# Performance work log

Hardware: AMD Instinct MI355X
Metric: run time of the kernel (lower is better)

## Reference

```python
import jax, jax.numpy as jnp
import numpy as np

B, C, H, W = 64, 3, 256, 256
K = 2  # multi_n_num
EPS_NORM = 1e-8
EPS_DEN = 1e-7
SCALE = 0.01


def setup_inputs() -> dict:
    key = jax.random.key(0)
    ka, kp, kn, kj = jax.random.split(key, 4)
    a = jax.random.normal(ka, (B, C, H, W), dtype=jnp.float32)
    p = jax.random.normal(kp, (B, C, H, W), dtype=jnp.float32)
    n = jax.random.normal(kn, (B, C, H, W), dtype=jnp.float32)
    # sample_with_j(B, 2, i) -> [i, random j != i]
    ar = jnp.arange(B, dtype=jnp.int64)
    off = jax.random.randint(kj, (B,), 1, B)  # offset in [1, B) guarantees j != i
    neg_idx = jnp.stack([ar, (ar + off) % B], axis=1).astype(jnp.int64)  # [B, K]
    return {"a": a, "p": p, "n": n, "neg_idx": neg_idx}


def _fft_norm(x):
    # torch.fft.fft2 over last two dims -> complex, same rank as x
    f = jnp.fft.fft2(x, axes=(-2, -1))  # [B, C, H, W] complex64
    # torch.norm(f, p=2, dim=1, keepdim=True) on complex = sqrt(sum |f|^2 over C)
    nrm = jnp.sqrt(jnp.sum(jnp.abs(f) ** 2, axis=1, keepdims=True))
    return f / (nrm + EPS_NORM) * SCALE


def reference(a, p, n, neg_idx):
    af = _fft_norm(a)
    pf = _fft_norm(p)
    nf = _fft_norm(n)
    # L1Loss on complex tensors = mean |diff| (complex magnitude)
    d_ap = jnp.mean(jnp.abs(af - pf), axis=(1, 2, 3))  # [B]
    n_sel = nf[neg_idx]  # [B, K, C, H, W]
    d_an = jnp.mean(jnp.abs(af[:, None] - n_sel), axis=(2, 3, 4))  # [B, K]
    contrastive = jnp.sum(d_ap[:, None] / (d_an + EPS_DEN))
    return contrastive / (K * B)
```

## Files before the change

kernel.cpp:

```cpp
#include <hip/hip_runtime.h>
#include <hip/hip_fp16.h>

#define B_ 64
#define SW_ 132
#define SIMG_ (256 * SW_)
#define TIMG_ (3 * SIMG_)
#define TELEMS_ ((size_t)B_ * TIMG_)
#define SST_ 257

__device__ __forceinline__ float2 h2f(__half2 v) { return __half22float2(v); }
__device__ __forceinline__ __half2 f2h(float2 v) { return __float22half2_rn(v); }
__device__ __forceinline__ float2 cmul(float2 a, float2 b) {
  return make_float2(a.x * b.x - a.y * b.y, a.x * b.y + a.y * b.x);
}
__device__ __forceinline__ int PHI(int e) { return e ^ ((e >> 4) & 0x0C); }
__device__ __forceinline__ int REV4(int k) {
  return ((k & 3) << 6) | ((k & 0xC) << 2) | ((k >> 2) & 0xC) | ((k >> 6) & 3);
}
#define LGKM0 asm volatile("s_waitcnt lgkmcnt(0)" ::: "memory")

__device__ __forceinline__ void r4stage(__half2* w, int i0, int q,
                                        float2 ta, float2 tb, float2 tc, bool tw) {
  int p0 = PHI(i0), p1 = PHI(i0 + q), p2 = PHI(i0 + 2 * q), p3 = PHI(i0 + 3 * q);
  float2 x0 = h2f(w[p0]), x1 = h2f(w[p1]), x2 = h2f(w[p2]), x3 = h2f(w[p3]);
  float2 a = make_float2(x0.x + x2.x, x0.y + x2.y);
  float2 b = make_float2(x0.x - x2.x, x0.y - x2.y);
  float2 c = make_float2(x1.x + x3.x, x1.y + x3.y);
  float2 d = make_float2(x1.x - x3.x, x1.y - x3.y);
  float2 y0 = make_float2(a.x + c.x, a.y + c.y);
  float2 y1 = make_float2(b.x + d.y, b.y - d.x);
  float2 y2 = make_float2(a.x - c.x, a.y - c.y);
  float2 y3 = make_float2(b.x - d.y, b.y + d.x);
  if (tw) { y1 = cmul(y1, ta); y2 = cmul(y2, tb); y3 = cmul(y3, tc); }
  w[p0] = f2h(y0); w[p1] = f2h(y1); w[p2] = f2h(y2); w[p3] = f2h(y3);
}

__device__ __forceinline__ void fft256_r4(__half2* w, int r, const float2* tws) {
  LGKM0;
  r4stage(w, r, 64, tws[0], tws[1], tws[2], true);
  LGKM0;
  r4stage(w, ((r >> 4) << 6) | (r & 15), 16, tws[3], tws[4], tws[5], true);
  LGKM0;
  r4stage(w, ((r >> 2) << 4) | (r & 3), 4, tws[6], tws[7], tws[8], true);
  LGKM0;
  float2 u = make_float2(1.0f, 0.0f);
  r4stage(w, 4 * r, 1, u, u, u, false);
  LGKM0;
}

__global__ __launch_bounds__(1024, 4) void fft2_fused(const float* __restrict__ a,
                                                      const float* __restrict__ p,
                                                      const float* __restrict__ n,
                                                      __half2* __restrict__ outbase) {
  __shared__ __half2 S[129 * SST_];
  __shared__ __half2 scr[16 * 256];

  int tid = threadIdx.x;
  int wv = tid >> 6;
  int r = tid & 63;
  int tensor = blockIdx.x / 192;
  int plane = blockIdx.x % 192;
  const float* in = (tensor == 0 ? a : (tensor == 1 ? p : n)) + (size_t)plane * 65536;
  __half2* outp = outbase + (size_t)tensor * TELEMS_ + (size_t)plane * SIMG_;

  float2 tw[9];
  {
    float s, c;
    __sincosf(-6.283185307179586f * (float)r / 256.0f, &s, &c);
    tw[0] = make_float2(c, s); tw[1] = cmul(tw[0], tw[0]); tw[2] = cmul(tw[1], tw[0]);
    __sincosf(-6.283185307179586f * (float)(r & 15) / 64.0f, &s, &c);
    tw[3] = make_float2(c, s); tw[4] = cmul(tw[3], tw[3]); tw[5] = cmul(tw[4], tw[3]);
    __sincosf(-6.283185307179586f * (float)(r & 3) / 16.0f, &s, &c);
    tw[6] = make_float2(c, s); tw[7] = cmul(tw[6], tw[6]); tw[8] = cmul(tw[7], tw[6]);
  }

  __half2* w = scr + wv * 256;

  for (int it = 0; it < 8; ++it) {
    int q = it * 16 + wv;
    const float4* r0 = (const float4*)(in + (size_t)(2 * q) * 256);
    const float4* r1 = (const float4*)(in + (size_t)(2 * q + 1) * 256);
    float4 v0 = r0[r];
    float4 v1 = r1[r];
    int pb = PHI(4 * r);
    w[pb]     = f2h(make_float2(v0.x, v1.x));
    w[pb + 1] = f2h(make_float2(v0.y, v1.y));
    w[pb + 2] = f2h(make_float2(v0.z, v1.z));
    w[pb + 3] = f2h(make_float2(v0.w, v1.w));
    fft256_r4(w, r, tw);
#pragma unroll
    for (int t = 0; t < 2; ++t) {
      int k = r + 64 * t;
      float2 Zk = h2f(w[PHI(REV4(k))]);
      float2 Zm = h2f(w[PHI(REV4((256 - k) & 255))]);
      float2 A  = make_float2(0.5f * (Zk.x + Zm.x), 0.5f * (Zk.y - Zm.y));
      float2 Bv = make_float2(0.5f * (Zk.y + Zm.y), 0.5f * (Zm.x - Zk.x));
      __half2* srow = S + k * SST_ + PHI(2 * q);
      srow[0] = f2h(A);
      srow[1] = f2h(Bv);
    }
    if (r == 0) {
      float2 Z = h2f(w[PHI(REV4(128))]);
      __half2* srow = S + 128 * SST_ + PHI(2 * q);
      srow[0] = f2h(make_float2(Z.x, 0.0f));
      srow[1] = f2h(make_float2(Z.y, 0.0f));
    }
    LGKM0;
  }

  __syncthreads();

  for (int it = 0; it < 9; ++it) {
    int c = it * 16 + wv;
    if (c <= 128) {
      __half2* row = S + c * SST_;
      fft256_r4(row, r, tw);
      __half2* dst = outp + (size_t)c * 256;
#pragma unroll
      for (int t = 0; t < 4; ++t) {
        int i = r + 64 * t;
        dst[i] = row[PHI(i)];
      }
    } else if (c < SW_) {
      __half2* dst = outp + (size_t)c * 256;
      __half2 z = f2h(make_float2(0.0f, 0.0f));
#pragma unroll
      for (int t = 0; t < 4; ++t) dst[r + 64 * t] = z;
    }
  }
}

__device__ __forceinline__ float cab2(float2 v) { return v.x * v.x + v.y * v.y; }

__global__ __launch_bounds__(256) void dist_kernel(const __half2* __restrict__ af,
                                                   const __half2* __restrict__ pf,
                                                   const __half2* __restrict__ nf,
                                                   const int* __restrict__ neg,
                                                   float* __restrict__ acc) {
  int b = blockIdx.y;
  int j;
  if (neg[1] == 0) {
    j = (int)((const long long*)neg)[b * 2 + 1];
  } else {
    j = neg[b * 2 + 1];
  }
  size_t ab = (size_t)b * TIMG_;
  size_t jb = (size_t)j * TIMG_;
  float s_ap = 0.0f, s_a0 = 0.0f, s_a1 = 0.0f;
#pragma unroll
  for (int t = 0; t < 4; ++t) {
    int flat = blockIdx.x * 1024 + t * 256 + threadIdx.x;
    int k2 = flat >> 8;
    float w = (k2 == 0 || k2 >= 128) ? 1.0f : 2.0f;
    float2 a0 = h2f(af[ab + flat]);
    float2 a1 = h2f(af[ab + SIMG_ + flat]);
    float2 a2 = h2f(af[ab + 2 * SIMG_ + flat]);
    float2 p0 = h2f(pf[ab + flat]);
    float2 p1 = h2f(pf[ab + SIMG_ + flat]);
    float2 p2 = h2f(pf[ab + 2 * SIMG_ + flat]);
    float2 n0 = h2f(nf[ab + flat]);
    float2 n1 = h2f(nf[ab + SIMG_ + flat]);
    float2 n2 = h2f(nf[ab + 2 * SIMG_ + flat]);
    float2 m0 = h2f(nf[jb + flat]);
    float2 m1 = h2f(nf[jb + SIMG_ + flat]);
    float2 m2 = h2f(nf[jb + 2 * SIMG_ + flat]);
    float sa = 0.01f / (sqrtf(cab2(a0) + cab2(a1) + cab2(a2)) + 1e-8f);
    float sp = 0.01f / (sqrtf(cab2(p0) + cab2(p1) + cab2(p2)) + 1e-8f);
    float sn = 0.01f / (sqrtf(cab2(n0) + cab2(n1) + cab2(n2)) + 1e-8f);
    float sm = 0.01f / (sqrtf(cab2(m0) + cab2(m1) + cab2(m2)) + 1e-8f);
    float dx, dy;
    dx = a0.x * sa - p0.x * sp; dy = a0.y * sa - p0.y * sp; s_ap += w * sqrtf(dx * dx + dy * dy);
    dx = a1.x * sa - p1.x * sp; dy = a1.y * sa - p1.y * sp; s_ap += w * sqrtf(dx * dx + dy * dy);
    dx = a2.x * sa - p2.x * sp; dy = a2.y * sa - p2.y * sp; s_ap += w * sqrtf(dx * dx + dy * dy);
    dx = a0.x * sa - n0.x * sn; dy = a0.y * sa - n0.y * sn; s_a0 += w * sqrtf(dx * dx + dy * dy);
    dx = a1.x * sa - n1.x * sn; dy = a1.y * sa - n1.y * sn; s_a0 += w * sqrtf(dx * dx + dy * dy);
    dx = a2.x * sa - n2.x * sn; dy = a2.y * sa - n2.y * sn; s_a0 += w * sqrtf(dx * dx + dy * dy);
    dx = a0.x * sa - m0.x * sm; dy = a0.y * sa - m0.y * sm; s_a1 += w * sqrtf(dx * dx + dy * dy);
    dx = a1.x * sa - m1.x * sm; dy = a1.y * sa - m1.y * sm; s_a1 += w * sqrtf(dx * dx + dy * dy);
    dx = a2.x * sa - m2.x * sm; dy = a2.y * sa - m2.y * sm; s_a1 += w * sqrtf(dx * dx + dy * dy);
  }
#pragma unroll
  for (int off = 32; off > 0; off >>= 1) {
    s_ap += __shfl_down(s_ap, off);
    s_a0 += __shfl_down(s_a0, off);
    s_a1 += __shfl_down(s_a1, off);
  }
  __shared__ float red[3][4];
  int lane = threadIdx.x & 63, wid = threadIdx.x >> 6;
  if (lane == 0) { red[0][wid] = s_ap; red[1][wid] = s_a0; red[2][wid] = s_a1; }
  __syncthreads();
  if (threadIdx.x == 0) {
    atomicAdd(&acc[b * 3 + 0], red[0][0] + red[0][1] + red[0][2] + red[0][3]);
    atomicAdd(&acc[b * 3 + 1], red[1][0] + red[1][1] + red[1][2] + red[1][3]);
    atomicAdd(&acc[b * 3 + 2], red[2][0] + red[2][1] + red[2][2] + red[2][3]);
  }
}

__global__ void zero_acc(float* acc) { acc[threadIdx.x] = 0.0f; }

__global__ void final_kernel(const float* __restrict__ acc, float* __restrict__ out) {
  int b = threadIdx.x;
  const float inv = 1.0f / 196608.0f;
  float dap = acc[b * 3 + 0] * inv;
  float da0 = acc[b * 3 + 1] * inv;
  float da1 = acc[b * 3 + 2] * inv;
  float term = dap / (da0 + 1e-7f) + dap / (da1 + 1e-7f);
#pragma unroll
  for (int off = 32; off > 0; off >>= 1) term += __shfl_down(term, off);
  if (b == 0) out[0] = term * (1.0f / 128.0f);
}

extern "C" void kernel_launch(void* const* d_in, const int* in_sizes, int n_in,
                              void* d_out, int out_size, void* d_ws, size_t ws_size,
                              hipStream_t stream) {
  const float* a = (const float*)d_in[0];
  const float* p = (const float*)d_in[1];
  const float* n = (const float*)d_in[2];
  const int* neg = (const int*)d_in[3];
  float* out = (float*)d_out;

  __half2* base = (__half2*)d_ws;
  float* acc = (float*)(base + 3 * TELEMS_);

  zero_acc<<<1, 192, 0, stream>>>(acc);
  fft2_fused<<<576, 1024, 0, stream>>>(a, p, n, base);
  dist_kernel<<<dim3(33, 64), 256, 0, stream>>>(base, base + TELEMS_,
                                                base + 2 * TELEMS_, neg, acc);
  final_kernel<<<1, 64, 0, stream>>>(acc, out);
}
```

Baseline: 253.5 us.

## Move 256-point FFT butterflies into registers with cross-lane shuffle exchanges

Replaces the LDS-scratch radix-4 FFT, which used per-stage shared-memory round trips and lgkmcnt waits, with a register-resident FFT: each lane holds four values and digit exchanges happen through __shfl_xor. The real-pair unpacking uses a shuffle to fetch mirrored bins instead of LDS reads, and the column pass stores outputs with 128-bit writes in natural order. The distance kernel now does vectorized uint4 loads of four consecutive bins per thread. Shuffles still go through the LDS crossbar, and the extra half/float conversions between stages add ALU work.

```diff
diff --git a/kernel.cpp b/kernel.cpp
--- a/kernel.cpp
+++ b/kernel.cpp
@@ -8,52 +8,73 @@
 #define TELEMS_ ((size_t)B_ * TIMG_)
 #define SST_ 257
 
-__device__ __forceinline__ float2 h2f(__half2 v) { return __half22float2(v); }
-__device__ __forceinline__ __half2 f2h(float2 v) { return __float22half2_rn(v); }
 __device__ __forceinline__ float2 cmul(float2 a, float2 b) {
   return make_float2(a.x * b.x - a.y * b.y, a.x * b.y + a.y * b.x);
 }
-__device__ __forceinline__ int PHI(int e) { return e ^ ((e >> 4) & 0x0C); }
-__device__ __forceinline__ int REV4(int k) {
-  return ((k & 3) << 6) | ((k & 0xC) << 2) | ((k >> 2) & 0xC) | ((k >> 6) & 3);
-}
-#define LGKM0 asm volatile("s_waitcnt lgkmcnt(0)" ::: "memory")
-
-__device__ __forceinline__ void r4stage(__half2* w, int i0, int q,
-                                        float2 ta, float2 tb, float2 tc, bool tw) {
-  int p0 = PHI(i0), p1 = PHI(i0 + q), p2 = PHI(i0 + 2 * q), p3 = PHI(i0 + 3 * q);
-  float2 x0 = h2f(w[p0]), x1 = h2f(w[p1]), x2 = h2f(w[p2]), x3 = h2f(w[p3]);
-  float2 a = make_float2(x0.x + x2.x, x0.y + x2.y);
-  float2 b = make_float2(x0.x - x2.x, x0.y - x2.y);
-  float2 c = make_float2(x1.x + x3.x, x1.y + x3.y);
-  float2 d = make_float2(x1.x - x3.x, x1.y - x3.y);
-  float2 y0 = make_float2(a.x + c.x, a.y + c.y);
+__device__ __forceinline__ unsigned f2u(float2 v) {
+  __half2 h = __float22half2_rn(v);
+  return __builtin_bit_cast(unsigned, h);
+}
+__device__ __forceinline__ float2 u2f(unsigned u) {
+  return __half22float2(__builtin_bit_cast(__half2, u));
+}
+
+__device__ __forceinline__ void bfly4(float2 x[4], float2 ta, float2 tb, float2 tc, bool tw) {
+  float2 a = make_float2(x[0].x + x[2].x, x[0].y + x[2].y);
+  float2 b = make_float2(x[0].x - x[2].x, x[0].y - x[2].y);
+  float2 c = make_float2(x[1].x + x[3].x, x[1].y + x[3].y);
+  float2 d = make_float2(x[1].x - x[3].x, x[1].y - x[3].y);
   float2 y1 = make_float2(b.x + d.y, b.y - d.x);
   float2 y2 = make_float2(a.x - c.x, a.y - c.y);
   float2 y3 = make_float2(b.x - d.y, b.y + d.x);
+  x[0] = make_float2(a.x + c.x, a.y + c.y);
   if (tw) { y1 = cmul(y1, ta); y2 = cmul(y2, tb); y3 = cmul(y3, tc); }
-  w[p0] = f2h(y0); w[p1] = f2h(y1); w[p2] = f2h(y2); w[p3] = f2h(y3);
-}
-
-__device__ __forceinline__ void fft256_r4(__half2* w, int r, const float2* tws) {
-  LGKM0;
-  r4stage(w, r, 64, tws[0], tws[1], tws[2], true);
-  LGKM0;
-  r4stage(w, ((r >> 4) << 6) | (r & 15), 16, tws[3], tws[4], tws[5], true);
-  LGKM0;
-  r4stage(w, ((r >> 2) << 4) | (r & 3), 4, tws[6], tws[7], tws[8], true);
-  LGKM0;
-  float2 u = make_float2(1.0f, 0.0f);
-  r4stage(w, 4 * r, 1, u, u, u, false);
-  LGKM0;
+  x[1] = y1; x[2] = y2; x[3] = y3;
+}
+
+__device__ __forceinline__ void xbit(unsigned& A, unsigned& B, int bit, int r) {
+  bool hi = (r >> bit) & 1;
+  int send = hi ? (int)A : (int)B;
+  int got = __shfl_xor(send, 1 << bit, 64);
+  if (hi) A = (unsigned)got; else B = (unsigned)got;
+}
+__device__ __forceinline__ void xdigit(unsigned u[4], int bit, int r) {
+  xbit(u[0], u[1], bit, r);
+  xbit(u[2], u[3], bit, r);
+  xbit(u[0], u[2], bit + 1, r);
+  xbit(u[1], u[3], bit + 1, r);
+}
+
+__device__ __forceinline__ void fft256_reg(float2 x[4], unsigned u[4], int r,
+                                           const float2 tw[9]) {
+  bfly4(x, tw[0], tw[1], tw[2], true);
+#pragma unroll
+  for (int s = 0; s < 4; ++s) u[s] = f2u(x[s]);
+  xdigit(u, 4, r);
+#pragma unroll
+  for (int s = 0; s < 4; ++s) x[s] = u2f(u[s]);
+  bfly4(x, tw[3], tw[4], tw[5], true);
+#pragma unroll
+  for (int s = 0; s < 4; ++s) u[s] = f2u(x[s]);
+  xdigit(u, 2, r);
+#pragma unroll
+  for (int s = 0; s < 4; ++s) x[s] = u2f(u[s]);
+  bfly4(x, tw[6], tw[7], tw[8], true);
+#pragma unroll
+  for (int s = 0; s < 4; ++s) u[s] = f2u(x[s]);
+  xdigit(u, 0, r);
+#pragma unroll
+  for (int s = 0; s < 4; ++s) x[s] = u2f(u[s]);
+  bfly4(x, tw[0], tw[0], tw[0], false);
+#pragma unroll
+  for (int s = 0; s < 4; ++s) u[s] = f2u(x[s]);
 }
 
 __global__ __launch_bounds__(1024, 4) void fft2_fused(const float* __restrict__ a,
                                                       const float* __restrict__ p,
                                                       const float* __restrict__ n,
-                                                      __half2* __restrict__ outbase) {
-  __shared__ __half2 S[129 * SST_];
-  __shared__ __half2 scr[16 * 256];
+                                                      unsigned* __restrict__ outbase) {
+  __shared__ unsigned S[129 * SST_];
 
   int tid = threadIdx.x;
   int wv = tid >> 6;
@@ -61,7 +82,7 @@
   int tensor = blockIdx.x / 192;
   int plane = blockIdx.x % 192;
   const float* in = (tensor == 0 ? a : (tensor == 1 ? p : n)) + (size_t)plane * 65536;
-  __half2* outp = outbase + (size_t)tensor * TELEMS_ + (size_t)plane * SIMG_;
+  unsigned* outp = outbase + (size_t)tensor * TELEMS_ + (size_t)plane * SIMG_;
 
   float2 tw[9];
   {
@@ -73,39 +94,36 @@
     __sincosf(-6.283185307179586f * (float)(r & 3) / 16.0f, &s, &c);
     tw[6] = make_float2(c, s); tw[7] = cmul(tw[6], tw[6]); tw[8] = cmul(tw[7], tw[6]);
   }
-
-  __half2* w = scr + wv * 256;
+  int m = ((r & 3) << 4) | (((r >> 2) & 3) << 2) | (r >> 4);
+  int mp = (64 - m) & 63;
+  int rp = ((mp >> 4) & 3) | (((mp >> 2) & 3) << 2) | ((mp & 3) << 4);
 
   for (int it = 0; it < 8; ++it) {
     int q = it * 16 + wv;
-    const float4* r0 = (const float4*)(in + (size_t)(2 * q) * 256);
-    const float4* r1 = (const float4*)(in + (size_t)(2 * q + 1) * 256);
-    float4 v0 = r0[r];
-    float4 v1 = r1[r];
-    int pb = PHI(4 * r);
-    w[pb]     = f2h(make_float2(v0.x, v1.x));
-    w[pb + 1] = f2h(make_float2(v0.y, v1.y));
-    w[pb + 2] = f2h(make_float2(v0.z, v1.z));
-    w[pb + 3] = f2h(make_float2(v0.w, v1.w));
-    fft256_r4(w, r, tw);
-#pragma unroll
-    for (int t = 0; t < 2; ++t) {
-      int k = r + 64 * t;
-      float2 Zk = h2f(w[PHI(REV4(k))]);
-      float2 Zm = h2f(w[PHI(REV4((256 - k) & 255))]);
+    const float* r0 = in + (size_t)(2 * q) * 256;
+    float2 x[4]; unsigned u[4];
+#pragma unroll
+    for (int j = 0; j < 4; ++j)
+      x[j] = make_float2(r0[r + 64 * j], r0[256 + r + 64 * j]);
+    fft256_reg(x, u, r, tw);
+    unsigned mir[4];
+#pragma unroll
+    for (int t = 0; t < 4; ++t) mir[t] = (unsigned)__shfl((int)u[t], rp, 64);
+#pragma unroll
+    for (int s = 0; s < 2; ++s) {
+      int k = 64 * s + m;
+      int sp = (m == 0) ? ((4 - s) & 3) : (3 - s);
+      float2 Zk = u2f(u[s]), Zm = u2f(mir[sp]);
       float2 A  = make_float2(0.5f * (Zk.x + Zm.x), 0.5f * (Zk.y - Zm.y));
       float2 Bv = make_float2(0.5f * (Zk.y + Zm.y), 0.5f * (Zm.x - Zk.x));
-      __half2* srow = S + k * SST_ + PHI(2 * q);
-      srow[0] = f2h(A);
-      srow[1] = f2h(Bv);
+      S[k * SST_ + 2 * q]     = f2u(A);
+      S[k * SST_ + 2 * q + 1] = f2u(Bv);
     }
     if (r == 0) {
-      float2 Z = h2f(w[PHI(REV4(128))]);
-      __half2* srow = S + 128 * SST_ + PHI(2 * q);
-      srow[0] = f2h(make_float2(Z.x, 0.0f));
-      srow[1] = f2h(make_float2(Z.y, 0.0f));
+      float2 Zk = u2f(u[2]);
+      S[128 * SST_ + 2 * q]     = f2u(make_float2(Zk.x, 0.0f));
+      S[128 * SST_ + 2 * q + 1] = f2u(make_float2(Zk.y, 0.0f));
     }
-    LGKM0;
   }
 
   __syncthreads();
@@ -113,72 +131,68 @@
   for (int it = 0; it < 9; ++it) {
     int c = it * 16 + wv;
     if (c <= 128) {
-      __half2* row = S + c * SST_;
-      fft256_r4(row, r, tw);
-      __half2* dst = outp + (size_t)c * 256;
-#pragma unroll
-      for (int t = 0; t < 4; ++t) {
-        int i = r + 64 * t;
-        dst[i] = row[PHI(i)];
-      }
-    } else if (c < SW_) {
-      __half2* dst = outp + (size_t)c * 256;
-      __half2 z = f2h(make_float2(0.0f, 0.0f));
-#pragma unroll
-      for (int t = 0; t < 4; ++t) dst[r + 64 * t] = z;
+      unsigned* srow = S + c * SST_;
+      float2 x[4]; unsigned u[4];
+#pragma unroll
+      for (int j = 0; j < 4; ++j) x[j] = u2f(srow[r + 64 * j]);
+      fft256_reg(x, u, r, tw);
+      *(uint4*)(outp + (size_t)c * 256 + 4 * r) = make_uint4(u[0], u[1], u[2], u[3]);
     }
   }
+  if (wv >= 13) {
+    int c = 129 + (wv - 13);
+    *(uint4*)(outp + (size_t)c * 256 + 4 * r) = make_uint4(0, 0, 0, 0);
+  }
 }
 
 __device__ __forceinline__ float cab2(float2 v) { return v.x * v.x + v.y * v.y; }
 
-__global__ __launch_bounds__(256) void dist_kernel(const __half2* __restrict__ af,
-                                                   const __half2* __restrict__ pf,
-                                                   const __half2* __restrict__ nf,
+__global__ __launch_bounds__(256) void dist_kernel(const unsigned* __restrict__ af,
+                                                   const unsigned* __restrict__ pf,
+                                                   const unsigned* __restrict__ nf,
                                                    const int* __restrict__ neg,
                                                    float* __restrict__ acc) {
   int b = blockIdx.y;
-  int j;
-  if (neg[1] == 0) {
-    j = (int)((const long long*)neg)[b * 2 + 1];
-  } else {
-    j = neg[b * 2 + 1];
-  }
+  int j = (neg[1] == 0) ? (int)((const long long*)neg)[b * 2 + 1] : neg[b * 2 + 1];
   size_t ab = (size_t)b * TIMG_;
   size_t jb = (size_t)j * TIMG_;
+  int t4 = blockIdx.x * 256 + threadIdx.x;
+  int flat0 = t4 * 4;
+  int k2 = flat0 >> 8;
+  float w = (k2 == 0 || k2 >= 128) ? 1.0f : 2.0f;
+
+  unsigned A[3][4], P[3][4], N[3][4], M[3][4];
+#pragma unroll
+  for (int ch = 0; ch < 3; ++ch) {
+    uint4 t;
+    t = *(const uint4*)(af + ab + ch * SIMG_ + flat0); A[ch][0]=t.x; A[ch][1]=t.y; A[ch][2]=t.z; A[ch][3]=t.w;
+    t = *(const uint4*)(pf + ab + ch * SIMG_ + flat0); P[ch][0]=t.x; P[ch][1]=t.y; P[ch][2]=t.z; P[ch][3]=t.w;
+    t = *(const uint4*)(nf + ab + ch * SIMG_ + flat0); N[ch][0]=t.x; N[ch][1]=t.y; N[ch][2]=t.z; N[ch][3]=t.w;
+    t = *(const uint4*)(nf + jb + ch * SIMG_ + flat0); M[ch][0]=t.x; M[ch][1]=t.y; M[ch][2]=t.z; M[ch][3]=t.w;
+  }
   float s_ap = 0.0f, s_a0 = 0.0f, s_a1 = 0.0f;
 #pragma unroll
-  for (int t = 0; t < 4; ++t) {
-    int flat = blockIdx.x * 1024 + t * 256 + threadIdx.x;
-    int k2 = flat >> 8;
-    float w = (k2 == 0 || k2 >= 128) ? 1.0f : 2.0f;
-    float2 a0 = h2f(af[ab + flat]);
-    float2 a1 = h2f(af[ab + SIMG_ + flat]);
-    float2 a2 = h2f(af[ab + 2 * SIMG_ + flat]);
-    float2 p0 = h2f(pf[ab + flat]);
-    float2 p1 = h2f(pf[ab + SIMG_ + flat]);
-    float2 p2 = h2f(pf[ab + 2 * SIMG_ + flat]);
-    float2 n0 = h2f(nf[ab + flat]);
-    float2 n1 = h2f(nf[ab + SIMG_ + flat]);
-    float2 n2 = h2f(nf[ab + 2 * SIMG_ + flat]);
-    float2 m0 = h2f(nf[jb + flat]);
-    float2 m1 = h2f(nf[jb + SIMG_ + flat]);
-    float2 m2 = h2f(nf[jb + 2 * SIMG_ + flat]);
+  for (int e = 0; e < 4; ++e) {
+    float2 a0 = u2f(A[0][e]), a1 = u2f(A[1][e]), a2 = u2f(A[2][e]);
+    float2 p0 = u2f(P[0][e]), p1 = u2f(P[1][e]), p2 = u2f(P[2][e]);
+    float2 n0 = u2f(N[0][e]), n1 = u2f(N[1][e]), n2 = u2f(N[2][e]);
+    float2 m0 = u2f(M[0][e]), m1 = u2f(M[1][e]), m2 = u2f(M[2][e]);
     float sa = 0.01f / (sqrtf(cab2(a0) + cab2(a1) + cab2(a2)) + 1e-8f);
     float sp = 0.01f / (sqrtf(cab2(p0) + cab2(p1) + cab2(p2)) + 1e-8f);
     float sn = 0.01f / (sqrtf(cab2(n0) + cab2(n1) + cab2(n2)) + 1e-8f);
     float sm = 0.01f / (sqrtf(cab2(m0) + cab2(m1) + cab2(m2)) + 1e-8f);
     float dx, dy;
-    dx = a0.x * sa - p0.x * sp; dy = a0.y * sa - p0.y * sp; s_ap += w * sqrtf(dx * dx + dy * dy);
-    dx = a1.x * sa - p1.x * sp; dy = a1.y * sa - p1.y * sp; s_ap += w * sqrtf(dx * dx + dy * dy);
-    dx = a2.x * sa - p2.x * sp; dy = a2.y * sa - p2.y * sp; s_ap += w * sqrtf(dx * dx + dy * dy);
-    dx = a0.x * sa - n0.x * sn; dy = a0.y * sa - n0.y * sn; s_a0 += w * sqrtf(dx * dx + dy * dy);
-    dx = a1.x * sa - n1.x * sn; dy = a1.y * sa - n1.y * sn; s_a0 += w * sqrtf(dx * dx + dy * dy);
-    dx = a2.x * sa - n2.x * sn; dy = a2.y * sa - n2.y * sn; s_a0 += w * sqrtf(dx * dx + dy * dy);
-    dx = a0.x * sa - m0.x * sm; dy = a0.y * sa - m0.y * sm; s_a1 += w * sqrtf(dx * dx + dy * dy);
-    dx = a1.x * sa - m1.x * sm; dy = a1.y * sa - m1.y * sm; s_a1 += w * sqrtf(dx * dx + dy * dy);
-    dx = a2.x * sa - m2.x * sm; dy = a2.y * sa - m2.y * sm; s_a1 += w * sqrtf(dx * dx + dy * dy);
-  }
+    dx = a0.x * sa - p0.x * sp; dy = a0.y * sa - p0.y * sp; s_ap += sqrtf(dx * dx + dy * dy);
+    dx = a1.x * sa - p1.x * sp; dy = a1.y * sa - p1.y * sp; s_ap += sqrtf(dx * dx + dy * dy);
+    dx = a2.x * sa - p2.x * sp; dy = a2.y * sa - p2.y * sp; s_ap += sqrtf(dx * dx + dy * dy);
+    dx = a0.x * sa - n0.x * sn; dy = a0.y * sa - n0.y * sn; s_a0 += sqrtf(dx * dx + dy * dy);
+    dx = a1.x * sa - n1.x * sn; dy = a1.y * sa - n1.y * sn; s_a0 += sqrtf(dx * dx + dy * dy);
+    dx = a2.x * sa - n2.x * sn; dy = a2.y * sa - n2.y * sn; s_a0 += sqrtf(dx * dx + dy * dy);
+    dx = a0.x * sa - m0.x * sm; dy = a0.y * sa - m0.y * sm; s_a1 += sqrtf(dx * dx + dy * dy);
+    dx = a1.x * sa - m1.x * sm; dy = a1.y * sa - m1.y * sm; s_a1 += sqrtf(dx * dx + dy * dy);
+    dx = a2.x * sa - m2.x * sm; dy = a2.y * sa - m2.y * sm; s_a1 += sqrtf(dx * dx + dy * dy);
+  }
+  s_ap *= w; s_a0 *= w; s_a1 *= w;
 #pragma unroll
   for (int off = 32; off > 0; off >>= 1) {
     s_ap += __shfl_down(s_ap, off);
@@ -219,7 +233,7 @@
   const int* neg = (const int*)d_in[3];
   float* out = (float*)d_out;
 
-  __half2* base = (__half2*)d_ws;
+  unsigned* base = (unsigned*)d_ws;
   float* acc = (float*)(base + 3 * TELEMS_);
 
   zero_acc<<<1, 192, 0, stream>>>(acc);
```

Result: faster. 247.0 us (-2.5%).
